# Kernel optimization log

Hardware: AMD Instinct MI355X
Metric: run time of the kernel (lower is better)

Reference implementation:

```python
import jax, jax.numpy as jnp
import numpy as np

B, C, U, LEN, K = 32, 16, 16, 128, 4  # batch, channels, units, image side, cheb order
POWERS = K + 1


def _path_chebyshev(n, k):
    """Chebyshev polynomials T_0..T_k of the rescaled normalized Laplacian of an
    undirected path graph with n nodes. Returns [k+1, n, n] float32."""
    A = np.zeros((n, n), dtype=np.float64)
    A[np.arange(n - 1), np.arange(1, n)] = 1.0
    A = A + A.T
    d = A.sum(axis=1)
    dinv = 1.0 / np.sqrt(d)
    L = np.eye(n) - dinv[:, None] * A * dinv[None, :]   # normalized Laplacian
    Lt = L - np.eye(n)                                   # rescaled: 2L/lambda_max - I, lambda_max=2
    T = [np.eye(n), Lt]
    for _ in range(2, k + 1):
        T.append(2.0 * Lt @ T[-1] - T[-2])
    return np.stack(T[: k + 1]).astype(np.float32)


def setup_inputs() -> dict:
    key = jax.random.key(0)
    kx, kc = jax.random.split(key)
    x = jax.random.normal(kx, (B, C, LEN, LEN), dtype=jnp.float32)
    coefs = 0.001 * jax.random.normal(kc, (POWERS, POWERS, C, U), dtype=jnp.float32)
    cheb = jnp.asarray(_path_chebyshev(LEN, K))  # same graph for both axes
    return {"x": x, "coefs": coefs, "cheb1": cheb, "cheb2": cheb}


def reference(x, coefs, cheb1, cheb2):
    # out[b,u,p,q] = sum_{k1,k2,c,h,w} coefs[k1,k2,c,u] * cheb1[k1,h,p] * x[b,c,h,w] * cheb2[k2,w,q]
    t1 = jnp.einsum('bchw,khp->bkcpw', x, cheb1)        # apply cheb1 along H
    s = jnp.einsum('bkcpw,klcu->blupw', t1, coefs)      # contract k1 and channels
    out = jnp.einsum('blupw,lwq->bupq', s, cheb2)       # apply cheb2 along W, contract k2
    return out
```

## Files before the change

### kernel.cpp

```cpp
#include <hip/hip_runtime.h>
#include <hip/hip_bf16.h>

#define LEN 128
#define NB 32
#define NC 16
#define NU 16
#define NK 5
#define KC 80
#define KCP 96

typedef unsigned int uint32;
typedef unsigned short ushort16;
typedef __attribute__((ext_vector_type(8))) short bf16x8;
typedef __attribute__((ext_vector_type(4))) float f32x4;

#define MFMA(a, b, c) __builtin_amdgcn_mfma_f32_16x16x32_bf16(a, b, c, 0, 0, 0)

#define SIG(r) (((r) & 15) ^ (((r) >> 3) & 15))

static __device__ inline ushort16 f2bf(float f) {
    union { float f; uint32 u; } v; v.f = f;
    uint32 u = v.u;
    uint32 r = (u + 0x7fffu + ((u >> 16) & 1u)) >> 16;
    return (ushort16)r;
}
static __device__ inline uint32 pkbf(float a, float b) {
    return (uint32)f2bf(a) | ((uint32)f2bf(b) << 16);
}
static __device__ inline bf16x8 frag16(const void* p) {
    return *(const bf16x8*)p;
}

__global__ __launch_bounds__(256) void k0_prep(const float* __restrict__ coefs,
                                               const float* __restrict__ cheb1,
                                               const float* __restrict__ cheb2,
                                               ushort16* __restrict__ cheb1F,
                                               ushort16* __restrict__ cheb2F,
                                               ushort16* __restrict__ coefF) {
    int i = blockIdx.x * 256 + threadIdx.x;
    if (i < 81920) {
        int j = i & 7, lane = (i >> 3) & 63, ks = (i >> 9) & 3, nt = i >> 11;
        int kp = nt * 16 + (lane & 15);
        int k = kp >> 7, p = kp & 127;
        int h = ks * 32 + ((lane >> 4) << 3) + j;
        cheb1F[i] = f2bf(cheb1[(k * LEN + h) * LEN + p]);
    } else if (i < 163840) {
        int i2 = i - 81920;
        int j = i2 & 7, lane = (i2 >> 3) & 63, t = i2 >> 9;
        int ks = t % 20, nt = t / 20;
        int q = nt * 16 + (lane & 15);
        int lw = ks * 32 + ((lane >> 4) << 3) + j;
        int l = lw >> 7, w = lw & 127;
        cheb2F[i2] = f2bf(cheb2[(l * LEN + w) * LEN + q]);
    } else if (i < 171520) {
        int i3 = i - 163840;
        int j = i3 & 7, lane = (i3 >> 3) & 63, t = i3 >> 9;
        int ks = t % 3, nt = t / 3;
        int lu = nt * 16 + (lane & 15);
        int l = lu >> 4, u = lu & 15;
        int kc = ks * 32 + ((lane >> 4) << 3) + j;
        int k = kc >> 4, c = kc & 15;
        coefF[i3] = (kc < KC) ? f2bf(coefs[((k * NK + l) * NC + c) * NU + u]) : (ushort16)0;
    }
}

__global__ __launch_bounds__(256) void kx_prep(const float* __restrict__ x,
                                               ushort16* __restrict__ xF) {
    __shared__ __align__(16) uint32 Xs[128 * 64];
    const int bc = blockIdx.x;
    const int tid = threadIdx.x;
    const float* xp = x + (size_t)bc * (LEN * LEN);
    {
        int w = tid & 127, hg = tid >> 7;
        #pragma unroll
        for (int uu = 0; uu < 8; ++uu) {
            int u = hg * 8 + uu;
            uint4 d;
            uint32* dp = (uint32*)&d;
            #pragma unroll
            for (int t = 0; t < 4; ++t) {
                int h2 = u * 4 + t;
                dp[t] = pkbf(xp[(2 * h2) * LEN + w], xp[(2 * h2 + 1) * LEN + w]);
            }
            *(uint4*)(Xs + w * 64 + ((u ^ SIG(w)) << 2)) = d;
        }
    }
    __syncthreads();
    ushort16* dst = xF + (size_t)bc * 16384;
    #pragma unroll
    for (int i = 0; i < 8; ++i) {
        int n = tid + i * 256;
        int lane = n & 63, fk = n >> 6;
        int wrow = (fk >> 2) * 16 + (lane & 15);
        int u = (fk & 3) * 4 + (lane >> 4);
        uint4 v = *(const uint4*)(Xs + wrow * 64 + ((u ^ SIG(wrow)) << 2));
        *(uint4*)(dst + (size_t)n * 8) = v;
    }
}

__global__ __launch_bounds__(256, 4) void k1_mfma(const ushort16* __restrict__ xF,
                                                  const ushort16* __restrict__ cheb1F,
                                                  ushort16* __restrict__ t1, int b0) {
    __shared__ __align__(16) uint32 Bs[80 * 64];
    const int c = blockIdx.x, bl = blockIdx.y, ns = blockIdx.z;
    const int b = b0 + bl;
    const int tid = threadIdx.x;
    const int lane = tid & 63, wm = tid >> 6;
    const int m16 = lane & 15, g = lane >> 4;

    const ushort16* xFb = xF + ((size_t)(b * NC + c)) * 16384;

    f32x4 acc[2][5];
    #pragma unroll
    for (int mi = 0; mi < 2; ++mi)
        #pragma unroll
        for (int ni = 0; ni < 5; ++ni) acc[mi][ni] = (f32x4)0.f;

    #pragma unroll
    for (int ks = 0; ks < 4; ++ks) {
        bf16x8 Af[2], Bf[5];
        #pragma unroll
        for (int mi = 0; mi < 2; ++mi) {
            int mt = wm * 2 + mi;
            Af[mi] = frag16(xFb + ((size_t)(mt * 4 + ks) * 64 + lane) * 8);
        }
        #pragma unroll
        for (int ni = 0; ni < 5; ++ni) {
            int nt = ns * 5 + ni;
            Bf[ni] = frag16(cheb1F + ((size_t)(nt * 4 + ks) * 64 + lane) * 8);
        }
        #pragma unroll
        for (int mi = 0; mi < 2; ++mi)
            #pragma unroll
            for (int ni = 0; ni < 5; ++ni)
                acc[mi][ni] = MFMA(Af[mi], Bf[ni], acc[mi][ni]);
    }

    #pragma unroll
    for (int ni = 0; ni < 5; ++ni)
        #pragma unroll
        for (int mi = 0; mi < 2; ++mi) {
            int rr = ni * 16 + m16;
            int wu = wm * 32 + mi * 16 + g * 4;
            uint2 d;
            d.x = pkbf(acc[mi][ni][0], acc[mi][ni][1]);
            d.y = pkbf(acc[mi][ni][2], acc[mi][ni][3]);
            int u = wu >> 3;
            *(uint2*)(Bs + rr * 64 + ((u ^ SIG(rr)) << 2) + ((wu >> 1) & 3)) = d;
        }
    __syncthreads();

    #pragma unroll
    for (int i = 0; i < 5; ++i) {
        int n = tid + i * 256;
        int rr = n >> 4, wsg = n & 15;
        uint4 v = *(const uint4*)(Bs + rr * 64 + ((wsg ^ SIG(rr)) << 2));
        int kp = ns * 80 + rr;
        int k = kp >> 7, p = kp & 127;
        *(uint4*)(t1 + ((size_t)((bl * LEN + p) * KC + k * NC + c)) * LEN + wsg * 8) = v;
    }
}

__global__ __launch_bounds__(256, 4) void k2_mfma(const ushort16* __restrict__ t1,
                                                  const ushort16* __restrict__ coefF,
                                                  const ushort16* __restrict__ cheb2F,
                                                  float* __restrict__ out, int b0) {
    __shared__ __align__(16) uint32 sm[128 * 64];
    const int p = blockIdx.x, bl = blockIdx.y, b = b0 + bl;
    const int tid = threadIdx.x;
    const int lane = tid & 63, wave = tid >> 6;
    const int n16 = lane & 15, g = lane >> 4;

    {
        const uint32* t1u = (const uint32*)(t1 + (size_t)(bl * LEN + p) * (KC * LEN));
        #pragma unroll
        for (int i = 0; i < 3; ++i) {
            int it = tid + i * 256;
            if (it < 640) {
                int a = it >> 4, wq = it & 15;
                const uint32* src = t1u + (2 * a) * 64 + wq * 4;
                uint4 Av = *(const uint4*)(src);
                uint4 Bv = *(const uint4*)(src + 64);
                const uint32* av = (const uint32*)&Av;
                const uint32* bv = (const uint32*)&Bv;
                int u = a >> 2, lo = a & 3;
                #pragma unroll
                for (int j = 0; j < 4; ++j) {
                    int r0 = wq * 8 + 2 * j, r1 = r0 + 1;
                    sm[r0 * 64 + ((u ^ SIG(r0)) << 2) + lo] = (av[j] & 0xffffu) | (bv[j] << 16);
                    sm[r1 * 64 + ((u ^ SIG(r1)) << 2) + lo] = (av[j] >> 16) | (bv[j] & 0xffff0000u);
                }
            }
        }
        #pragma unroll
        for (int i = 0; i < 4; ++i) {
            int idx = tid + i * 256;
            int row = idx >> 3, d = idx & 7;
            int u = 10 + (d >> 2);
            sm[row * 64 + ((u ^ SIG(row)) << 2) + (d & 3)] = 0;
        }
    }
    __syncthreads();

    f32x4 acc[2][5];
    #pragma unroll
    for (int mi = 0; mi < 2; ++mi)
        #pragma unroll
        for (int ni = 0; ni < 5; ++ni) acc[mi][ni] = (f32x4)0.f;

    #pragma unroll
    for (int ks = 0; ks < 3; ++ks) {
        bf16x8 Af[2], Bf[5];
        #pragma unroll
        for (int mi = 0; mi < 2; ++mi) {
            int row = wave * 32 + mi * 16 + n16;
            int uu = ks * 4 + g;
            Af[mi] = frag16(sm + row * 64 + ((uu ^ SIG(row)) << 2));
        }
        #pragma unroll
        for (int ni = 0; ni < 5; ++ni)
            Bf[ni] = frag16(coefF + ((size_t)(ni * 3 + ks) * 64 + lane) * 8);
        #pragma unroll
        for (int mi = 0; mi < 2; ++mi)
            #pragma unroll
            for (int ni = 0; ni < 5; ++ni)
                acc[mi][ni] = MFMA(Af[mi], Bf[ni], acc[mi][ni]);
    }
    __syncthreads();

    {
        ushort16* A3 = (ushort16*)sm;
        #pragma unroll
        for (int mi = 0; mi < 2; ++mi)
            #pragma unroll
            for (int ni = 0; ni < 5; ++ni) {
                int wcol = wave * 32 + mi * 16 + g * 4;
                uint2 d;
                d.x = pkbf(acc[mi][ni][0], acc[mi][ni][1]);
                d.y = pkbf(acc[mi][ni][2], acc[mi][ni][3]);
                *(uint2*)(A3 + n16 * 648 + ni * 128 + wcol) = d;
            }
    }
    __syncthreads();

    const ushort16* A3r = (const ushort16*)sm;
    f32x4 c3[2];
    c3[0] = (f32x4)0.f; c3[1] = (f32x4)0.f;
    #pragma unroll 5
    for (int ks = 0; ks < 20; ++ks) {
        bf16x8 Aa = frag16(A3r + n16 * 648 + ks * 32 + g * 8);
        #pragma unroll
        for (int nt = 0; nt < 2; ++nt) {
            bf16x8 Bb = frag16(cheb2F + ((size_t)((wave * 2 + nt) * 20 + ks) * 64 + lane) * 8);
            c3[nt] = MFMA(Aa, Bb, c3[nt]);
        }
    }

    #pragma unroll
    for (int nt = 0; nt < 2; ++nt)
        #pragma unroll
        for (int r = 0; r < 4; ++r) {
            int u = g * 4 + r;
            int q = wave * 32 + nt * 16 + n16;
            out[(((size_t)(b * NU + u)) * LEN + p) * LEN + q] = c3[nt][r];
        }
}

extern "C" void kernel_launch(void* const* d_in, const int* in_sizes, int n_in,
                              void* d_out, int out_size, void* d_ws, size_t ws_size,
                              hipStream_t stream) {
    const float* x     = (const float*)d_in[0];
    const float* coefs = (const float*)d_in[1];
    const float* cheb1 = (const float*)d_in[2];
    const float* cheb2 = (const float*)d_in[3];
    float* out = (float*)d_out;

    const size_t xF_bytes  = (size_t)NB * NC * 16384 * sizeof(ushort16);
    const size_t aux_bytes = 163840 + 163840 + 15360;
    size_t off = (ws_size - aux_bytes - xF_bytes) & ~(size_t)255;
    ushort16* cheb1F = (ushort16*)((char*)d_ws + off);
    ushort16* cheb2F = cheb1F + 81920;
    ushort16* coefF  = cheb2F + 81920;
    ushort16* xF     = coefF + 7680;
    ushort16* t1 = (ushort16*)d_ws;

    const size_t per_b = (size_t)LEN * KC * LEN * sizeof(ushort16);
    int chunk = (int)(off / per_b);
    if (chunk < 1) chunk = 1;
    if (chunk > NB) chunk = NB;

    hipLaunchKernelGGL(k0_prep, dim3(171520 / 256), dim3(256), 0, stream,
                       coefs, cheb1, cheb2, cheb1F, cheb2F, coefF);
    hipLaunchKernelGGL(kx_prep, dim3(NB * NC), dim3(256), 0, stream, x, xF);
    for (int b0 = 0; b0 < NB; b0 += chunk) {
        int cb = (NB - b0 < chunk) ? (NB - b0) : chunk;
        hipLaunchKernelGGL(k1_mfma, dim3(NC, cb, 8), dim3(256), 0, stream,
                           xF, cheb1F, t1, b0);
        hipLaunchKernelGGL(k2_mfma, dim3(LEN, cb), dim3(256), 0, stream,
                           t1, coefF, cheb2F, out, b0);
    }
}
```

Baseline: 151.0 us.

## Merge prep kernels and give k1/k2 blocks two output tiles each for reuse

Fuses the two preprocessing kernels into one launch. k1 now loads its x fragments once and computes two N-slices per block, halving the grid. k2 handles two p rows per block, prefetching the second row's t1 data into registers while the first row's MFMAs run, and its final GEMM uses two A tiles against each cheb2 fragment. The aim is to reuse cheb2/coef fragments and cut launch count, at the cost of more registers (launch bound lowered to 3), a larger shared buffer and half as many blocks.

```diff
diff --git a/kernel.cpp b/kernel.cpp
--- a/kernel.cpp
+++ b/kernel.cpp
@@ -31,70 +31,71 @@
     return *(const bf16x8*)p;
 }
 
-__global__ __launch_bounds__(256) void k0_prep(const float* __restrict__ coefs,
-                                               const float* __restrict__ cheb1,
-                                               const float* __restrict__ cheb2,
-                                               ushort16* __restrict__ cheb1F,
-                                               ushort16* __restrict__ cheb2F,
-                                               ushort16* __restrict__ coefF) {
-    int i = blockIdx.x * 256 + threadIdx.x;
-    if (i < 81920) {
-        int j = i & 7, lane = (i >> 3) & 63, ks = (i >> 9) & 3, nt = i >> 11;
-        int kp = nt * 16 + (lane & 15);
-        int k = kp >> 7, p = kp & 127;
-        int h = ks * 32 + ((lane >> 4) << 3) + j;
-        cheb1F[i] = f2bf(cheb1[(k * LEN + h) * LEN + p]);
-    } else if (i < 163840) {
-        int i2 = i - 81920;
-        int j = i2 & 7, lane = (i2 >> 3) & 63, t = i2 >> 9;
-        int ks = t % 20, nt = t / 20;
-        int q = nt * 16 + (lane & 15);
-        int lw = ks * 32 + ((lane >> 4) << 3) + j;
-        int l = lw >> 7, w = lw & 127;
-        cheb2F[i2] = f2bf(cheb2[(l * LEN + w) * LEN + q]);
-    } else if (i < 171520) {
-        int i3 = i - 163840;
-        int j = i3 & 7, lane = (i3 >> 3) & 63, t = i3 >> 9;
-        int ks = t % 3, nt = t / 3;
-        int lu = nt * 16 + (lane & 15);
-        int l = lu >> 4, u = lu & 15;
-        int kc = ks * 32 + ((lane >> 4) << 3) + j;
-        int k = kc >> 4, c = kc & 15;
-        coefF[i3] = (kc < KC) ? f2bf(coefs[((k * NK + l) * NC + c) * NU + u]) : (ushort16)0;
-    }
-}
-
-__global__ __launch_bounds__(256) void kx_prep(const float* __restrict__ x,
-                                               ushort16* __restrict__ xF) {
+__global__ __launch_bounds__(256) void kprep(const float* __restrict__ x,
+                                             const float* __restrict__ coefs,
+                                             const float* __restrict__ cheb1,
+                                             const float* __restrict__ cheb2,
+                                             ushort16* __restrict__ xF,
+                                             ushort16* __restrict__ cheb1F,
+                                             ushort16* __restrict__ cheb2F,
+                                             ushort16* __restrict__ coefF) {
     __shared__ __align__(16) uint32 Xs[128 * 64];
-    const int bc = blockIdx.x;
-    const int tid = threadIdx.x;
-    const float* xp = x + (size_t)bc * (LEN * LEN);
-    {
-        int w = tid & 127, hg = tid >> 7;
-        #pragma unroll
-        for (int uu = 0; uu < 8; ++uu) {
-            int u = hg * 8 + uu;
-            uint4 d;
-            uint32* dp = (uint32*)&d;
-            #pragma unroll
-            for (int t = 0; t < 4; ++t) {
-                int h2 = u * 4 + t;
-                dp[t] = pkbf(xp[(2 * h2) * LEN + w], xp[(2 * h2 + 1) * LEN + w]);
-            }
-            *(uint4*)(Xs + w * 64 + ((u ^ SIG(w)) << 2)) = d;
-        }
-    }
-    __syncthreads();
-    ushort16* dst = xF + (size_t)bc * 16384;
-    #pragma unroll
-    for (int i = 0; i < 8; ++i) {
-        int n = tid + i * 256;
-        int lane = n & 63, fk = n >> 6;
-        int wrow = (fk >> 2) * 16 + (lane & 15);
-        int u = (fk & 3) * 4 + (lane >> 4);
-        uint4 v = *(const uint4*)(Xs + wrow * 64 + ((u ^ SIG(wrow)) << 2));
-        *(uint4*)(dst + (size_t)n * 8) = v;
+    const int blk = blockIdx.x, tid = threadIdx.x;
+    if (blk < 512) {
+        const int bc = blk;
+        const float* xp = x + (size_t)bc * (LEN * LEN);
+        {
+            int w = tid & 127, hg = tid >> 7;
+            #pragma unroll
+            for (int uu = 0; uu < 8; ++uu) {
+                int u = hg * 8 + uu;
+                uint4 d;
+                uint32* dp = (uint32*)&d;
+                #pragma unroll
+                for (int t = 0; t < 4; ++t) {
+                    int h2 = u * 4 + t;
+                    dp[t] = pkbf(xp[(2 * h2) * LEN + w], xp[(2 * h2 + 1) * LEN + w]);
+                }
+                *(uint4*)(Xs + w * 64 + ((u ^ SIG(w)) << 2)) = d;
+            }
+        }
+        __syncthreads();
+        ushort16* dst = xF + (size_t)bc * 16384;
+        #pragma unroll
+        for (int i = 0; i < 8; ++i) {
+            int n = tid + i * 256;
+            int lane = n & 63, fk = n >> 6;
+            int wrow = (fk >> 2) * 16 + (lane & 15);
+            int u = (fk & 3) * 4 + (lane >> 4);
+            uint4 v = *(const uint4*)(Xs + wrow * 64 + ((u ^ SIG(wrow)) << 2));
+            *(uint4*)(dst + (size_t)n * 8) = v;
+        }
+    } else {
+        int i = (blk - 512) * 256 + tid;
+        if (i < 81920) {
+            int j = i & 7, lane = (i >> 3) & 63, ks = (i >> 9) & 3, nt = i >> 11;
+            int kp = nt * 16 + (lane & 15);
+            int k = kp >> 7, p = kp & 127;
+            int h = ks * 32 + ((lane >> 4) << 3) + j;
+            cheb1F[i] = f2bf(cheb1[(k * LEN + h) * LEN + p]);
+        } else if (i < 163840) {
+            int i2 = i - 81920;
+            int j = i2 & 7, lane = (i2 >> 3) & 63, t = i2 >> 9;
+            int ks = t % 20, nt = t / 20;
+            int q = nt * 16 + (lane & 15);
+            int lw = ks * 32 + ((lane >> 4) << 3) + j;
+            int l = lw >> 7, w = lw & 127;
+            cheb2F[i2] = f2bf(cheb2[(l * LEN + w) * LEN + q]);
+        } else {
+            int i3 = i - 163840;
+            int j = i3 & 7, lane = (i3 >> 3) & 63, t = i3 >> 9;
+            int ks = t % 3, nt = t / 3;
+            int lu = nt * 16 + (lane & 15);
+            int l = lu >> 4, u = lu & 15;
+            int kc = ks * 32 + ((lane >> 4) << 3) + j;
+            int k = kc >> 4, c = kc & 15;
+            coefF[i3] = (kc < KC) ? f2bf(coefs[((k * NK + l) * NC + c) * NU + u]) : (ushort16)0;
+        }
     }
 }
 
@@ -102,7 +103,7 @@
                                                   const ushort16* __restrict__ cheb1F,
                                                   ushort16* __restrict__ t1, int b0) {
     __shared__ __align__(16) uint32 Bs[80 * 64];
-    const int c = blockIdx.x, bl = blockIdx.y, ns = blockIdx.z;
+    const int c = blockIdx.x, bl = blockIdx.y, nsp = blockIdx.z;
     const int b = b0 + bl;
     const int tid = threadIdx.x;
     const int lane = tid & 63, wm = tid >> 6;
@@ -110,103 +111,130 @@
 
     const ushort16* xFb = xF + ((size_t)(b * NC + c)) * 16384;
 
-    f32x4 acc[2][5];
+    bf16x8 Af[2][4];
     #pragma unroll
     for (int mi = 0; mi < 2; ++mi)
         #pragma unroll
-        for (int ni = 0; ni < 5; ++ni) acc[mi][ni] = (f32x4)0.f;
-
-    #pragma unroll
-    for (int ks = 0; ks < 4; ++ks) {
-        bf16x8 Af[2], Bf[5];
-        #pragma unroll
-        for (int mi = 0; mi < 2; ++mi) {
+        for (int ks = 0; ks < 4; ++ks) {
             int mt = wm * 2 + mi;
-            Af[mi] = frag16(xFb + ((size_t)(mt * 4 + ks) * 64 + lane) * 8);
-        }
-        #pragma unroll
-        for (int ni = 0; ni < 5; ++ni) {
-            int nt = ns * 5 + ni;
-            Bf[ni] = frag16(cheb1F + ((size_t)(nt * 4 + ks) * 64 + lane) * 8);
-        }
-        #pragma unroll
-        for (int mi = 0; mi < 2; ++mi)
+            Af[mi][ks] = frag16(xFb + ((size_t)(mt * 4 + ks) * 64 + lane) * 8);
+        }
+
+    #pragma unroll
+    for (int s2 = 0; s2 < 2; ++s2) {
+        const int ns = nsp * 2 + s2;
+        f32x4 acc[2][5];
+        #pragma unroll
+        for (int mi = 0; mi < 2; ++mi)
+            #pragma unroll
+            for (int ni = 0; ni < 5; ++ni) acc[mi][ni] = (f32x4)0.f;
+
+        #pragma unroll
+        for (int ks = 0; ks < 4; ++ks) {
+            bf16x8 Bf[5];
             #pragma unroll
             for (int ni = 0; ni < 5; ++ni)
-                acc[mi][ni] = MFMA(Af[mi], Bf[ni], acc[mi][ni]);
-    }
-
-    #pragma unroll
-    for (int ni = 0; ni < 5; ++ni)
-        #pragma unroll
-        for (int mi = 0; mi < 2; ++mi) {
-            int rr = ni * 16 + m16;
-            int wu = wm * 32 + mi * 16 + g * 4;
-            uint2 d;
-            d.x = pkbf(acc[mi][ni][0], acc[mi][ni][1]);
-            d.y = pkbf(acc[mi][ni][2], acc[mi][ni][3]);
-            int u = wu >> 3;
-            *(uint2*)(Bs + rr * 64 + ((u ^ SIG(rr)) << 2) + ((wu >> 1) & 3)) = d;
-        }
-    __syncthreads();
-
-    #pragma unroll
-    for (int i = 0; i < 5; ++i) {
-        int n = tid + i * 256;
-        int rr = n >> 4, wsg = n & 15;
-        uint4 v = *(const uint4*)(Bs + rr * 64 + ((wsg ^ SIG(rr)) << 2));
-        int kp = ns * 80 + rr;
-        int k = kp >> 7, p = kp & 127;
-        *(uint4*)(t1 + ((size_t)((bl * LEN + p) * KC + k * NC + c)) * LEN + wsg * 8) = v;
-    }
-}
-
-__global__ __launch_bounds__(256, 4) void k2_mfma(const ushort16* __restrict__ t1,
+                Bf[ni] = frag16(cheb1F + ((size_t)((ns * 5 + ni) * 4 + ks) * 64 + lane) * 8);
+            #pragma unroll
+            for (int mi = 0; mi < 2; ++mi)
+                #pragma unroll
+                for (int ni = 0; ni < 5; ++ni)
+                    acc[mi][ni] = MFMA(Af[mi][ks], Bf[ni], acc[mi][ni]);
+        }
+
+        if (s2) __syncthreads();
+
+        #pragma unroll
+        for (int ni = 0; ni < 5; ++ni)
+            #pragma unroll
+            for (int mi = 0; mi < 2; ++mi) {
+                int rr = ni * 16 + m16;
+                int wu = wm * 32 + mi * 16 + g * 4;
+                uint2 d;
+                d.x = pkbf(acc[mi][ni][0], acc[mi][ni][1]);
+                d.y = pkbf(acc[mi][ni][2], acc[mi][ni][3]);
+                int u = wu >> 3;
+                *(uint2*)(Bs + rr * 64 + ((u ^ SIG(rr)) << 2) + ((wu >> 1) & 3)) = d;
+            }
+        __syncthreads();
+
+        #pragma unroll
+        for (int i = 0; i < 5; ++i) {
+            int n = tid + i * 256;
+            int rr = n >> 4, wsg = n & 15;
+            uint4 v = *(const uint4*)(Bs + rr * 64 + ((wsg ^ SIG(rr)) << 2));
+            int kp = ns * 80 + rr;
+            int k = kp >> 7, p = kp & 127;
+            *(uint4*)(t1 + ((size_t)((bl * LEN + p) * KC + k * NC + c)) * LEN + wsg * 8) = v;
+        }
+    }
+}
+
+__global__ __launch_bounds__(256, 3) void k2_mfma(const ushort16* __restrict__ t1,
                                                   const ushort16* __restrict__ coefF,
                                                   const ushort16* __restrict__ cheb2F,
                                                   float* __restrict__ out, int b0) {
-    __shared__ __align__(16) uint32 sm[128 * 64];
-    const int p = blockIdx.x, bl = blockIdx.y, b = b0 + bl;
+    __shared__ __align__(16) uint32 sm[10368];
+    const int pg = blockIdx.x, bl = blockIdx.y, b = b0 + bl;
     const int tid = threadIdx.x;
     const int lane = tid & 63, wave = tid >> 6;
     const int n16 = lane & 15, g = lane >> 4;
 
-    {
-        const uint32* t1u = (const uint32*)(t1 + (size_t)(bl * LEN + p) * (KC * LEN));
-        #pragma unroll
-        for (int i = 0; i < 3; ++i) {
-            int it = tid + i * 256;
-            if (it < 640) {
-                int a = it >> 4, wq = it & 15;
-                const uint32* src = t1u + (2 * a) * 64 + wq * 4;
-                uint4 Av = *(const uint4*)(src);
-                uint4 Bv = *(const uint4*)(src + 64);
-                const uint32* av = (const uint32*)&Av;
-                const uint32* bv = (const uint32*)&Bv;
-                int u = a >> 2, lo = a & 3;
-                #pragma unroll
-                for (int j = 0; j < 4; ++j) {
-                    int r0 = wq * 8 + 2 * j, r1 = r0 + 1;
-                    sm[r0 * 64 + ((u ^ SIG(r0)) << 2) + lo] = (av[j] & 0xffffu) | (bv[j] << 16);
-                    sm[r1 * 64 + ((u ^ SIG(r1)) << 2) + lo] = (av[j] >> 16) | (bv[j] & 0xffff0000u);
-                }
-            }
-        }
-        #pragma unroll
-        for (int i = 0; i < 4; ++i) {
-            int idx = tid + i * 256;
-            int row = idx >> 3, d = idx & 7;
-            int u = 10 + (d >> 2);
-            sm[row * 64 + ((u ^ SIG(row)) << 2) + (d & 3)] = 0;
-        }
-    }
-    __syncthreads();
-
-    f32x4 acc[2][5];
-    #pragma unroll
-    for (int mi = 0; mi < 2; ++mi)
-        #pragma unroll
-        for (int ni = 0; ni < 5; ++ni) acc[mi][ni] = (f32x4)0.f;
+    for (int j = tid; j < 2048; j += 256) {
+        int row = j >> 3, d = j & 7;
+        int u = 10 + (d >> 2);
+        sm[row * 64 + ((u ^ SIG(row)) << 2) + (d & 3)] = 0;
+    }
+
+    const uint32* t1base = (const uint32*)(t1 + (size_t)(bl * LEN + 2 * pg) * (KC * LEN));
+
+    uint4 Av[3], Bv[3];
+    f32x4 acc[2][2][5];
+    #pragma unroll
+    for (int pi = 0; pi < 2; ++pi)
+        #pragma unroll
+        for (int mi = 0; mi < 2; ++mi)
+            #pragma unroll
+            for (int ni = 0; ni < 5; ++ni) acc[pi][mi][ni] = (f32x4)0.f;
+
+    #pragma unroll
+    for (int i = 0; i < 3; ++i) {
+        int it = tid + i * 256;
+        if (it < 640) {
+            int a2 = it >> 4, wq = it & 15;
+            const uint32* src = t1base + a2 * 128 + wq * 4;
+            Av[i] = *(const uint4*)(src);
+            Bv[i] = *(const uint4*)(src + 64);
+        }
+    }
+    #pragma unroll
+    for (int i = 0; i < 3; ++i) {
+        int it = tid + i * 256;
+        if (it < 640) {
+            int a2 = it >> 4, wq = it & 15;
+            const uint32* av = (const uint32*)&Av[i];
+            const uint32* bv = (const uint32*)&Bv[i];
+            int u = a2 >> 2, lo = a2 & 3;
+            #pragma unroll
+            for (int j = 0; j < 4; ++j) {
+                int r0 = wq * 8 + 2 * j, r1 = r0 + 1;
+                sm[r0 * 64 + ((u ^ SIG(r0)) << 2) + lo] = (av[j] & 0xffffu) | (bv[j] << 16);
+                sm[r1 * 64 + ((u ^ SIG(r1)) << 2) + lo] = (av[j] >> 16) | (bv[j] & 0xffff0000u);
+            }
+        }
+    }
+    __syncthreads();
+
+    #pragma unroll
+    for (int i = 0; i < 3; ++i) {
+        int it = tid + i * 256;
+        if (it < 640) {
+            int a2 = it >> 4, wq = it & 15;
+            const uint32* src = t1base + 5120 + a2 * 128 + wq * 4;
+            Av[i] = *(const uint4*)(src);
+            Bv[i] = *(const uint4*)(src + 64);
+        }
+    }
 
     #pragma unroll
     for (int ks = 0; ks < 3; ++ks) {
@@ -214,8 +242,7 @@
         #pragma unroll
         for (int mi = 0; mi < 2; ++mi) {
             int row = wave * 32 + mi * 16 + n16;
-            int uu = ks * 4 + g;
-            Af[mi] = frag16(sm + row * 64 + ((uu ^ SIG(row)) << 2));
+            Af[mi] = frag16(sm + row * 64 + (((ks * 4 + g) ^ SIG(row)) << 2));
         }
         #pragma unroll
         for (int ni = 0; ni < 5; ++ni)
@@ -224,46 +251,95 @@
         for (int mi = 0; mi < 2; ++mi)
             #pragma unroll
             for (int ni = 0; ni < 5; ++ni)
-                acc[mi][ni] = MFMA(Af[mi], Bf[ni], acc[mi][ni]);
+                acc[0][mi][ni] = MFMA(Af[mi], Bf[ni], acc[0][mi][ni]);
+    }
+    __syncthreads();
+
+    #pragma unroll
+    for (int i = 0; i < 3; ++i) {
+        int it = tid + i * 256;
+        if (it < 640) {
+            int a2 = it >> 4, wq = it & 15;
+            const uint32* av = (const uint32*)&Av[i];
+            const uint32* bv = (const uint32*)&Bv[i];
+            int u = a2 >> 2, lo = a2 & 3;
+            #pragma unroll
+            for (int j = 0; j < 4; ++j) {
+                int r0 = wq * 8 + 2 * j, r1 = r0 + 1;
+                sm[r0 * 64 + ((u ^ SIG(r0)) << 2) + lo] = (av[j] & 0xffffu) | (bv[j] << 16);
+                sm[r1 * 64 + ((u ^ SIG(r1)) << 2) + lo] = (av[j] >> 16) | (bv[j] & 0xffff0000u);
+            }
+        }
+    }
+    __syncthreads();
+
+    #pragma unroll
+    for (int ks = 0; ks < 3; ++ks) {
+        bf16x8 Af[2], Bf[5];
+        #pragma unroll
+        for (int mi = 0; mi < 2; ++mi) {
+            int row = wave * 32 + mi * 16 + n16;
+            Af[mi] = frag16(sm + row * 64 + (((ks * 4 + g) ^ SIG(row)) << 2));
+        }
+        #pragma unroll
+        for (int ni = 0; ni < 5; ++ni)
+            Bf[ni] = frag16(coefF + ((size_t)(ni * 3 + ks) * 64 + lane) * 8);
+        #pragma unroll
+        for (int mi = 0; mi < 2; ++mi)
+            #pragma unroll
+            for (int ni = 0; ni < 5; ++ni)
+                acc[1][mi][ni] = MFMA(Af[mi], Bf[ni], acc[1][mi][ni]);
     }
     __syncthreads();
 
     {
         ushort16* A3 = (ushort16*)sm;
         #pragma unroll
-        for (int mi = 0; mi < 2; ++mi)
-            #pragma unroll
-            for (int ni = 0; ni < 5; ++ni) {
-                int wcol = wave * 32 + mi * 16 + g * 4;
-                uint2 d;
-                d.x = pkbf(acc[mi][ni][0], acc[mi][ni][1]);
-                d.y = pkbf(acc[mi][ni][2], acc[mi][ni][3]);
-                *(uint2*)(A3 + n16 * 648 + ni * 128 + wcol) = d;
-            }
+        for (int pi = 0; pi < 2; ++pi)
+            #pragma unroll
+            for (int mi = 0; mi < 2; ++mi)
+                #pragma unroll
+                for (int ni = 0; ni < 5; ++ni) {
+                    int wcol = wave * 32 + mi * 16 + g * 4;
+                    int row = pi * 16 + n16;
+                    uint2 d;
+                    d.x = pkbf(acc[pi][mi][ni][0], acc[pi][mi][ni][1]);
+                    d.y = pkbf(acc[pi][mi][ni][2], acc[pi][mi][ni][3]);
+                    *(uint2*)((ushort16*)sm + row * 648 + ni * 128 + wcol) = d;
+                }
     }
     __syncthreads();
 
     const ushort16* A3r = (const ushort16*)sm;
-    f32x4 c3[2];
-    c3[0] = (f32x4)0.f; c3[1] = (f32x4)0.f;
+    f32x4 c3[2][2];
+    c3[0][0] = (f32x4)0.f; c3[0][1] = (f32x4)0.f;
+    c3[1][0] = (f32x4)0.f; c3[1][1] = (f32x4)0.f;
     #pragma unroll 5
     for (int ks = 0; ks < 20; ++ks) {
-        bf16x8 Aa = frag16(A3r + n16 * 648 + ks * 32 + g * 8);
-        #pragma unroll
-        for (int nt = 0; nt < 2; ++nt) {
-            bf16x8 Bb = frag16(cheb2F + ((size_t)((wave * 2 + nt) * 20 + ks) * 64 + lane) * 8);
-            c3[nt] = MFMA(Aa, Bb, c3[nt]);
-        }
-    }
-
-    #pragma unroll
-    for (int nt = 0; nt < 2; ++nt)
-        #pragma unroll
-        for (int r = 0; r < 4; ++r) {
-            int u = g * 4 + r;
-            int q = wave * 32 + nt * 16 + n16;
-            out[(((size_t)(b * NU + u)) * LEN + p) * LEN + q] = c3[nt][r];
-        }
+        bf16x8 Af2[2], Bf2[2];
+        #pragma unroll
+        for (int mi = 0; mi < 2; ++mi)
+            Af2[mi] = frag16(A3r + (mi * 16 + n16) * 648 + ks * 32 + g * 8);
+        #pragma unroll
+        for (int nt = 0; nt < 2; ++nt)
+            Bf2[nt] = frag16(cheb2F + ((size_t)((wave * 2 + nt) * 20 + ks) * 64 + lane) * 8);
+        #pragma unroll
+        for (int mi = 0; mi < 2; ++mi)
+            #pragma unroll
+            for (int nt = 0; nt < 2; ++nt)
+                c3[mi][nt] = MFMA(Af2[mi], Bf2[nt], c3[mi][nt]);
+    }
+
+    #pragma unroll
+    for (int mi = 0; mi < 2; ++mi)
+        #pragma unroll
+        for (int nt = 0; nt < 2; ++nt)
+            #pragma unroll
+            for (int r = 0; r < 4; ++r) {
+                int u = g * 4 + r;
+                int q = wave * 32 + nt * 16 + n16;
+                out[(((size_t)(b * NU + u)) * LEN + (2 * pg + mi)) * LEN + q] = c3[mi][nt][r];
+            }
 }
 
 extern "C" void kernel_launch(void* const* d_in, const int* in_sizes, int n_in,
@@ -288,15 +364,16 @@
     int chunk = (int)(off / per_b);
     if (chunk < 1) chunk = 1;
     if (chunk > NB) chunk = NB;
-
-    hipLaunchKernelGGL(k0_prep, dim3(171520 / 256), dim3(256), 0, stream,
-                       coefs, cheb1, cheb2, cheb1F, cheb2F, coefF);
-    hipLaunchKernelGGL(kx_prep, dim3(NB * NC), dim3(256), 0, stream, x, xF);
+    chunk &= ~1;
+    if (chunk < 2) chunk = 2;
+
+    hipLaunchKernelGGL(kprep, dim3(1182), dim3(256), 0, stream,
+                       x, coefs, cheb1, cheb2, xF, cheb1F, cheb2F, coefF);
     for (int b0 = 0; b0 < NB; b0 += chunk) {
         int cb = (NB - b0 < chunk) ? (NB - b0) : chunk;
-        hipLaunchKernelGGL(k1_mfma, dim3(NC, cb, 8), dim3(256), 0, stream,
+        hipLaunchKernelGGL(k1_mfma, dim3(NC, cb, 4), dim3(256), 0, stream,
                            xF, cheb1F, t1, b0);
-        hipLaunchKernelGGL(k2_mfma, dim3(LEN, cb), dim3(256), 0, stream,
+        hipLaunchKernelGGL(k2_mfma, dim3(64, cb), dim3(256), 0, stream,
                            t1, coefF, cheb2F, out, b0);
     }
 }
```

After: 151.0 us. About the same (+0.0%).
